# Performance work log

Measured on AMD Instinct MI355X. Metric: run time of the kernel, lower is better.

## Reference

```python
import jax, jax.numpy as jnp
import numpy as np

N_NODES = 25000
N_EDGES = 400000
N_GRAPHS = 64
F_IN = 128


def setup_inputs() -> dict:
    key = jax.random.key(0)
    ks = jax.random.split(key, 16)
    inp = {}
    inp["x"] = jax.random.normal(ks[0], (N_NODES, F_IN), dtype=jnp.float32)
    inp["edge_index"] = jax.random.randint(ks[1], (2, N_EDGES), 0, N_NODES, dtype=jnp.int64)
    inp["edge_attr"] = jax.random.uniform(ks[2], (N_EDGES,), dtype=jnp.float32)
    inp["batch_ids"] = jnp.sort(jax.random.randint(ks[3], (N_NODES,), 0, N_GRAPHS, dtype=jnp.int64))
    def lin(k, fan_in, fan_out):
        bound = 1.0 / np.sqrt(fan_in)
        return jax.random.uniform(k, (fan_in, fan_out), dtype=jnp.float32, minval=-bound, maxval=bound)
    inp["W1_rel"] = lin(ks[4], F_IN, 512)
    inp["b1"] = jnp.zeros((512,), jnp.float32)
    inp["W1_root"] = lin(ks[5], F_IN, 512)
    inp["W2_rel"] = lin(ks[6], 512, 512)
    inp["b2"] = jnp.zeros((512,), jnp.float32)
    inp["W2_root"] = lin(ks[7], 512, 512)
    inp["Wl1"] = lin(ks[8], 512, 64)
    inp["bl1"] = jnp.zeros((64,), jnp.float32)
    inp["Wl2"] = lin(ks[9], 64, 16)
    inp["bl2"] = jnp.zeros((16,), jnp.float32)
    inp["Wl3"] = lin(ks[10], 16, 1)
    inp["bl3"] = jnp.zeros((1,), jnp.float32)
    return inp


def _graph_conv(h, src, dst, edge_attr, W_rel, b_rel, W_root, n_nodes):
    # PyG GraphConv: lin_rel(scatter_add(w_e * x_src, dst)) + lin_root(x)
    msg = h[src] * edge_attr[:, None]                       # [E, F] gather
    agg = jax.ops.segment_sum(msg, dst, num_segments=n_nodes)  # [N, F] scatter-add
    return agg @ W_rel + b_rel + h @ W_root


def reference(x, edge_index, edge_attr, batch_ids, W1_rel, b1, W1_root,
              W2_rel, b2, W2_root, Wl1, bl1, Wl2, bl2, Wl3, bl3):
    n_nodes = x.shape[0]
    src, dst = edge_index[0], edge_index[1]
    h = jax.nn.relu(_graph_conv(x, src, dst, edge_attr, W1_rel, b1, W1_root, n_nodes))
    h = jax.nn.relu(_graph_conv(h, src, dst, edge_attr, W2_rel, b2, W2_root, n_nodes))
    # global mean pool by graph id
    sums = jax.ops.segment_sum(h, batch_ids, num_segments=N_GRAPHS)  # [G, 512]
    counts = jax.ops.segment_sum(jnp.ones((n_nodes,), h.dtype), batch_ids, num_segments=N_GRAPHS)
    g = sums / jnp.maximum(counts, 1.0)[:, None]
    # dropout is identity in eval mode
    g = jax.nn.relu(g @ Wl1 + bl1)
    g = jax.nn.relu(g @ Wl2 + bl2)
    return g @ Wl3 + bl3  # [G, 1]
```

## Files before the change

### kernel.cpp

```cpp
#include <hip/hip_runtime.h>
#include <hip/hip_bf16.h>
#include <hip/hip_fp16.h>
#include <stdint.h>

#define N_NODESC 25000
#define N_EDGESC 400000
#define N_GRAPHSC 64
#define F_INC 128
#define HIDC 512
#define PSTRIDE 1600000

typedef __attribute__((ext_vector_type(8))) short short8;
typedef __attribute__((ext_vector_type(4))) float f32x4;

__device__ __forceinline__ float bf2f(unsigned short u) {
  return __uint_as_float(((unsigned)u) << 16);
}
__device__ __forceinline__ unsigned short f2bf(float f) {
  unsigned u = __float_as_uint(f);
  u += 0x7fffu + ((u >> 16) & 1u);
  return (unsigned short)(u >> 16);
}

__global__ void prep_kernel(const float* __restrict__ x, unsigned short* __restrict__ xp,
                            int* __restrict__ deg, float* __restrict__ gsum) {
  int blk = blockIdx.x, t = threadIdx.x;
  if (blk < 98) {
    int i = blk * 256 + t;
    if (i < N_NODESC) deg[i] = 0;
  } else if (blk < 3223) {
    int idx = ((blk - 98) * 256 + t) * 4;
    int node = idx >> 7;
    int col = idx & 127;
    float4 v = *(const float4*)(x + idx);
    ushort4 o;
    o.x = f2bf(v.x); o.y = f2bf(v.y); o.z = f2bf(v.z); o.w = f2bf(v.w);
    *(ushort4*)(xp + (size_t)(col >> 6) * PSTRIDE + (size_t)node * 64 + (col & 63)) = o;
  } else {
    int i = (blk - 3223) * 256 + t;
    if (i < N_GRAPHSC * HIDC) gsum[i] = 0.f;
  }
}

__global__ __launch_bounds__(256)
void wt_kernel(const float* __restrict__ W1rel, const float* __restrict__ W1root,
               const float* __restrict__ W2rel, const float* __restrict__ W2root,
               unsigned short* __restrict__ W1T, unsigned short* __restrict__ W2T) {
  __shared__ float tile[64][65];
  int blk = blockIdx.x;
  const float* src;
  unsigned short* dst;
  int n0, k0, Kout;
  if (blk < 128) {
    int kt = blk >> 3, nt = blk & 7;
    k0 = kt * 64; n0 = nt * 64;
    src = (k0 < 512) ? (W2rel + (size_t)k0 * 512) : (W2root + (size_t)(k0 - 512) * 512);
    dst = W2T; Kout = 1024;
  } else {
    int b = blk - 128;
    int kt = b >> 3, nt = b & 7;
    k0 = kt * 64; n0 = nt * 64;
    src = (k0 < 128) ? (W1rel + (size_t)k0 * 512) : (W1root + (size_t)(k0 - 128) * 512);
    dst = W1T; Kout = 256;
  }
  int c = threadIdx.x & 63;
  int r4 = threadIdx.x >> 6;
#pragma unroll
  for (int rr = 0; rr < 64; rr += 4) {
    int row = rr + r4;
    tile[c][row] = src[(size_t)row * 512 + n0 + c];
  }
  __syncthreads();
#pragma unroll
  for (int rr = 0; rr < 64; rr += 4) {
    int nrow = rr + r4;
    dst[(size_t)(n0 + nrow) * Kout + k0 + c] = f2bf(tile[nrow][c]);
  }
}

__global__ void deg_kernel(const int* __restrict__ ei, int* __restrict__ deg) {
  int e = blockIdx.x * blockDim.x + threadIdx.x;
  if (e >= N_EDGESC) return;
  atomicAdd(&deg[ei[N_EDGESC + e]], 1);
}

__global__ __launch_bounds__(1024)
void scan_kernel(const int* __restrict__ deg, int* __restrict__ indptr, int* __restrict__ cursor) {
  __shared__ int sums[1024];
  const int t = threadIdx.x;
  const int CH = (N_NODESC + 1023) / 1024;
  const int base = t * CH;
  int s = 0;
  for (int i = 0; i < CH; ++i) {
    int idx = base + i;
    if (idx < N_NODESC) s += deg[idx];
  }
  sums[t] = s;
  __syncthreads();
  for (int off = 1; off < 1024; off <<= 1) {
    int v = (t >= off) ? sums[t - off] : 0;
    __syncthreads();
    sums[t] += v;
    __syncthreads();
  }
  int run = (t > 0) ? sums[t - 1] : 0;
  for (int i = 0; i < CH; ++i) {
    int idx = base + i;
    if (idx < N_NODESC) {
      indptr[idx] = run;
      cursor[idx] = run;
      run += deg[idx];
    }
  }
  if (t == 0) indptr[N_NODESC] = sums[1023];
}

__global__ void fill_kernel(const int* __restrict__ ei, const float* __restrict__ ea,
                            int* __restrict__ cursor, unsigned* __restrict__ emeta) {
  int e = blockIdx.x * blockDim.x + threadIdx.x;
  if (e >= N_EDGESC) return;
  int dst = ei[N_EDGESC + e];
  int pos = atomicAdd(&cursor[dst], 1);
  unsigned short hw = __half_as_ushort(__float2half_rn(ea[e]));
  emeta[pos] = (unsigned)ei[e] | ((unsigned)hw << 16);
}

__global__ __launch_bounds__(256)
void agg_gather_p(const unsigned short* __restrict__ srcfeat, const int* __restrict__ indptr,
                  const unsigned* __restrict__ emeta, unsigned short* __restrict__ outp,
                  int lgP) {
  int P1 = (1 << lgP) - 1;
  int panel = blockIdx.x & P1;
  int node = (blockIdx.x >> lgP) * 4 + (threadIdx.x >> 6);
  if (node >= N_NODESC) return;
  int lane = threadIdx.x & 63;
  int q = lane >> 4;
  int c16 = lane & 15;
  int beg = indptr[node], end = indptr[node + 1];
  const unsigned short* fb = srcfeat + (size_t)panel * PSTRIDE + c16 * 4;
  float a0 = 0.f, a1 = 0.f, a2 = 0.f, a3 = 0.f;
  for (int b = beg; b < end; b += 64) {
    int cnt = end - b;
    if (cnt > 64) cnt = 64;
    unsigned mj = (lane < cnt) ? emeta[b + lane] : 0u;
    for (int j = 0; j < cnt; j += 8) {
      unsigned m0 = __shfl(mj, j + q);
      unsigned m1 = __shfl(mj, j + 4 + q);
      uint2 v0 = *(const uint2*)(fb + (size_t)(m0 & 0xffffu) * 64);
      uint2 v1 = *(const uint2*)(fb + (size_t)(m1 & 0xffffu) * 64);
      float w0 = __half2float(__ushort_as_half((unsigned short)(m0 >> 16)));
      float w1 = __half2float(__ushort_as_half((unsigned short)(m1 >> 16)));
      a0 += __uint_as_float(v0.x << 16) * w0;
      a1 += __uint_as_float(v0.x & 0xffff0000u) * w0;
      a2 += __uint_as_float(v0.y << 16) * w0;
      a3 += __uint_as_float(v0.y & 0xffff0000u) * w0;
      a0 += __uint_as_float(v1.x << 16) * w1;
      a1 += __uint_as_float(v1.x & 0xffff0000u) * w1;
      a2 += __uint_as_float(v1.y << 16) * w1;
      a3 += __uint_as_float(v1.y & 0xffff0000u) * w1;
    }
  }
  a0 += __shfl_xor(a0, 16); a1 += __shfl_xor(a1, 16);
  a2 += __shfl_xor(a2, 16); a3 += __shfl_xor(a3, 16);
  a0 += __shfl_xor(a0, 32); a1 += __shfl_xor(a1, 32);
  a2 += __shfl_xor(a2, 32); a3 += __shfl_xor(a3, 32);
  if (q == 0) {
    ushort4 o;
    o.x = f2bf(a0); o.y = f2bf(a1); o.z = f2bf(a2); o.w = f2bf(a3);
    *(ushort4*)(outp + (size_t)panel * PSTRIDE + (size_t)node * 64 + c16 * 4) = o;
  }
}

__global__ __launch_bounds__(256, 3)
void gemm_bt_relu(const short* __restrict__ A0, const short* __restrict__ A1,
                  const short* __restrict__ BT, const float* __restrict__ bias,
                  unsigned short* __restrict__ Outp, int M, int S) {
  const int K = 2 * S;
  __shared__ __align__(16) short As[128 * 64];
  __shared__ __align__(16) short Bs[128 * 64];
  const int m0 = blockIdx.x * 128;
  const int n0 = blockIdx.y * 128;
  const int tid = threadIdx.x;
  const int wave = tid >> 6;
  const int lane = tid & 63;
  const int quad = lane >> 4;
  const int r = lane & 15;
  const int wm = (wave >> 1) * 64;
  const int wn = (wave & 1) * 64;

  f32x4 acc[4][4] = {};

  const int nk = K >> 6;
  for (int kt = 0; kt < nk; ++kt) {
    const int kbase = kt << 6;
    const short* Ab;
    int koff;
    if (kbase < S) { Ab = A0; koff = kbase; } else { Ab = A1; koff = kbase - S; }
    const short* Apan = Ab + (size_t)(koff >> 6) * PSTRIDE;
#pragma unroll
    for (int i = 0; i < 4; ++i) {
      int s = ((wave * 4 + i) << 6) + lane;
      int row = s >> 3;
      int c = (s & 7) ^ (row & 7);
      int rg = m0 + row; if (rg > M - 1) rg = M - 1;
      const short* gp = Apan + (size_t)rg * 64 + (c << 3);
      __builtin_amdgcn_global_load_lds((const __attribute__((address_space(1))) void*)gp,
                                       (__attribute__((address_space(3))) void*)&As[(wave * 4 + i) * 512],
                                       16, 0, 0);
    }
#pragma unroll
    for (int i = 0; i < 4; ++i) {
      int s = ((wave * 4 + i) << 6) + lane;
      int row = s >> 3;
      int c = (s & 7) ^ (row & 7);
      const short* gp = BT + (size_t)(n0 + row) * K + kbase + (c << 3);
      __builtin_amdgcn_global_load_lds((const __attribute__((address_space(1))) void*)gp,
                                       (__attribute__((address_space(3))) void*)&Bs[(wave * 4 + i) * 512],
                                       16, 0, 0);
    }
    __syncthreads();
#pragma unroll
    for (int ks = 0; ks < 2; ++ks) {
      short8 af[4], bfr[4];
#pragma unroll
      for (int tm = 0; tm < 4; ++tm) {
        int ml = wm + tm * 16 + r;
        int c = (ks << 2) + quad;
        int slot = ml * 8 + (c ^ (ml & 7));
        af[tm] = *(const short8*)&As[slot * 8];
      }
#pragma unroll
      for (int tn = 0; tn < 4; ++tn) {
        int nl = wn + tn * 16 + r;
        int c = (ks << 2) + quad;
        int slot = nl * 8 + (c ^ (nl & 7));
        bfr[tn] = *(const short8*)&Bs[slot * 8];
      }
#pragma unroll
      for (int tm = 0; tm < 4; ++tm)
#pragma unroll
        for (int tn = 0; tn < 4; ++tn)
          acc[tm][tn] = __builtin_amdgcn_mfma_f32_16x16x32_bf16(af[tm], bfr[tn], acc[tm][tn], 0, 0, 0);
    }
    __syncthreads();
  }

#pragma unroll
  for (int tm = 0; tm < 4; ++tm) {
    int rowb = m0 + wm + tm * 16 + quad * 4;
#pragma unroll
    for (int tn = 0; tn < 4; ++tn) {
      int col = n0 + wn + tn * 16 + r;
      float bv = bias[col];
      unsigned short* obase = Outp + (size_t)(col >> 6) * PSTRIDE + (col & 63);
#pragma unroll
      for (int reg = 0; reg < 4; ++reg) {
        int rr = rowb + reg;
        if (rr < M) {
          float v = acc[tm][tn][reg] + bv;
          v = v > 0.f ? v : 0.f;
          obase[(size_t)rr * 64] = f2bf(v);
        }
      }
    }
  }
}

__global__ __launch_bounds__(256, 3)
void gemm_bt_pool(const short* __restrict__ A0, const short* __restrict__ A1,
                  const short* __restrict__ BT, const float* __restrict__ bias,
                  const int* __restrict__ batch, float* __restrict__ gsum, int M, int S) {
  const int K = 2 * S;
  __shared__ __align__(16) short As[128 * 64];
  __shared__ __align__(16) short Bs[128 * 64];
  const int m0 = blockIdx.x * 128;
  const int n0 = blockIdx.y * 128;
  const int tid = threadIdx.x;
  const int wave = tid >> 6;
  const int lane = tid & 63;
  const int quad = lane >> 4;
  const int r = lane & 15;
  const int wm = (wave >> 1) * 64;
  const int wn = (wave & 1) * 64;

  f32x4 acc[4][4] = {};

  const int nk = K >> 6;
  for (int kt = 0; kt < nk; ++kt) {
    const int kbase = kt << 6;
    const short* Ab;
    int koff;
    if (kbase < S) { Ab = A0; koff = kbase; } else { Ab = A1; koff = kbase - S; }
    const short* Apan = Ab + (size_t)(koff >> 6) * PSTRIDE;
#pragma unroll
    for (int i = 0; i < 4; ++i) {
      int s = ((wave * 4 + i) << 6) + lane;
      int row = s >> 3;
      int c = (s & 7) ^ (row & 7);
      int rg = m0 + row; if (rg > M - 1) rg = M - 1;
      const short* gp = Apan + (size_t)rg * 64 + (c << 3);
      __builtin_amdgcn_global_load_lds((const __attribute__((address_space(1))) void*)gp,
                                       (__attribute__((address_space(3))) void*)&As[(wave * 4 + i) * 512],
                                       16, 0, 0);
    }
#pragma unroll
    for (int i = 0; i < 4; ++i) {
      int s = ((wave * 4 + i) << 6) + lane;
      int row = s >> 3;
      int c = (s & 7) ^ (row & 7);
      const short* gp = BT + (size_t)(n0 + row) * K + kbase + (c << 3);
      __builtin_amdgcn_global_load_lds((const __attribute__((address_space(1))) void*)gp,
                                       (__attribute__((address_space(3))) void*)&Bs[(wave * 4 + i) * 512],
                                       16, 0, 0);
    }
    __syncthreads();
#pragma unroll
    for (int ks = 0; ks < 2; ++ks) {
      short8 af[4], bfr[4];
#pragma unroll
      for (int tm = 0; tm < 4; ++tm) {
        int ml = wm + tm * 16 + r;
        int c = (ks << 2) + quad;
        int slot = ml * 8 + (c ^ (ml & 7));
        af[tm] = *(const short8*)&As[slot * 8];
      }
#pragma unroll
      for (int tn = 0; tn < 4; ++tn) {
        int nl = wn + tn * 16 + r;
        int c = (ks << 2) + quad;
        int slot = nl * 8 + (c ^ (nl & 7));
        bfr[tn] = *(const short8*)&Bs[slot * 8];
      }
#pragma unroll
      for (int tm = 0; tm < 4; ++tm)
#pragma unroll
        for (int tn = 0; tn < 4; ++tn)
          acc[tm][tn] = __builtin_amdgcn_mfma_f32_16x16x32_bf16(af[tm], bfr[tn], acc[tm][tn], 0, 0, 0);
    }
    __syncthreads();
  }

  int gid[4][4];
#pragma unroll
  for (int tm = 0; tm < 4; ++tm) {
    int rowb = m0 + wm + tm * 16 + quad * 4;
#pragma unroll
    for (int reg = 0; reg < 4; ++reg) {
      int rr = rowb + reg;
      gid[tm][reg] = batch[rr < M ? rr : (M - 1)];
    }
#pragma unroll
    for (int tn = 0; tn < 4; ++tn) {
      float bv = bias[n0 + wn + tn * 16 + r];
#pragma unroll
      for (int reg = 0; reg < 4; ++reg) {
        int rr = rowb + reg;
        float v = acc[tm][tn][reg] + bv;
        v = v > 0.f ? v : 0.f;
        acc[tm][tn][reg] = (rr < M) ? v : 0.f;
      }
    }
  }
  int g_lo = batch[m0 < M ? m0 : (M - 1)];
  int g_hi = batch[(m0 + 127) < M ? (m0 + 127) : (M - 1)];
  for (int g = g_lo; g <= g_hi; ++g) {
#pragma unroll
    for (int tn = 0; tn < 4; ++tn) {
      float s = 0.f;
#pragma unroll
      for (int tm = 0; tm < 4; ++tm)
#pragma unroll
        for (int reg = 0; reg < 4; ++reg)
          s += (gid[tm][reg] == g) ? acc[tm][tn][reg] : 0.f;
      s += __shfl_xor(s, 16);
      s += __shfl_xor(s, 32);
      if (quad == 0)
        atomicAdd(&gsum[(size_t)g * HIDC + n0 + wn + tn * 16 + r], s);
    }
  }
}

__global__ __launch_bounds__(256)
void mlp_kernel(const float* __restrict__ gsum, const int* __restrict__ batch,
                const float* __restrict__ Wl1, const float* __restrict__ bl1,
                const float* __restrict__ Wl2, const float* __restrict__ bl2,
                const float* __restrict__ Wl3, const float* __restrict__ bl3,
                float* __restrict__ out) {
  int gi = blockIdx.x;
  int t = threadIdx.x;
  int unit = t & 63;
  int part = t >> 6;
  __shared__ float red[4][64];
  __shared__ float h1s[64];
  __shared__ float h2s[16];
  int lo = 0, hi = N_NODESC;
  while (lo < hi) { int mid = (lo + hi) >> 1; if (batch[mid] < gi) lo = mid + 1; else hi = mid; }
  int start = lo;
  hi = N_NODESC;
  while (lo < hi) { int mid = (lo + hi) >> 1; if (batch[mid] < gi + 1) lo = mid + 1; else hi = mid; }
  float inv = 1.0f / fmaxf((float)(lo - start), 1.0f);
  const float* gr = gsum + gi * HIDC;
  float acc = 0.f;
  for (int j = part * 128; j < (part + 1) * 128; ++j)
    acc += gr[j] * Wl1[j * 64 + unit];
  red[part][unit] = acc;
  __syncthreads();
  if (t < 64) {
    float a = bl1[t] + (red[0][t] + red[1][t] + red[2][t] + red[3][t]) * inv;
    h1s[t] = fmaxf(a, 0.f);
  }
  __syncthreads();
  if (t < 16) {
    float a = bl2[t];
    for (int j = 0; j < 64; ++j) a += h1s[j] * Wl2[j * 16 + t];
    h2s[t] = fmaxf(a, 0.f);
  }
  __syncthreads();
  if (t == 0) {
    float a = bl3[0];
    for (int j = 0; j < 16; ++j) a += h2s[j] * Wl3[j];
    out[gi] = a;
  }
}

extern "C" void kernel_launch(void* const* d_in, const int* in_sizes, int n_in,
                              void* d_out, int out_size, void* d_ws, size_t ws_size,
                              hipStream_t stream) {
  const float* x      = (const float*)d_in[0];
  const int*   ei     = (const int*)d_in[1];
  const float* ea     = (const float*)d_in[2];
  const int*   batch  = (const int*)d_in[3];
  const float* W1rel  = (const float*)d_in[4];
  const float* b1     = (const float*)d_in[5];
  const float* W1root = (const float*)d_in[6];
  const float* W2rel  = (const float*)d_in[7];
  const float* b2     = (const float*)d_in[8];
  const float* W2root = (const float*)d_in[9];
  const float* Wl1    = (const float*)d_in[10];
  const float* bl1    = (const float*)d_in[11];
  const float* Wl2    = (const float*)d_in[12];
  const float* bl2    = (const float*)d_in[13];
  const float* Wl3    = (const float*)d_in[14];
  const float* bl3    = (const float*)d_in[15];
  float* out = (float*)d_out;

  char* ws = (char*)d_ws;
  unsigned short* xp     = (unsigned short*)(ws + 0);
  unsigned short* agg1p  = (unsigned short*)(ws + 6400000);
  unsigned short* h1p    = (unsigned short*)(ws + 12800000);
  unsigned short* agg2p  = (unsigned short*)(ws + 38400000);
  unsigned short* W1T    = (unsigned short*)(ws + 64000000);
  unsigned short* W2T    = (unsigned short*)(ws + 64262144);
  float*          gsum   = (float*)(ws + 65310720);
  int*            deg    = (int*)(ws + 65441792);
  int*            cursor = (int*)(ws + 65541792);
  int*            indptr = (int*)(ws + 65641792);
  unsigned*       emeta  = (unsigned*)(ws + 65741808);

  prep_kernel<<<3351, 256, 0, stream>>>(x, xp, deg, gsum);
  wt_kernel<<<160, 256, 0, stream>>>(W1rel, W1root, W2rel, W2root, W1T, W2T);
  deg_kernel<<<(N_EDGESC + 255) / 256, 256, 0, stream>>>(ei, deg);
  scan_kernel<<<1, 1024, 0, stream>>>(deg, indptr, cursor);
  fill_kernel<<<(N_EDGESC + 255) / 256, 256, 0, stream>>>(ei, ea, cursor, emeta);

  agg_gather_p<<<((N_NODESC + 3) / 4) * 2, 256, 0, stream>>>(xp, indptr, emeta, agg1p, 1);

  dim3 gg((N_NODESC + 127) / 128, 4);
  gemm_bt_relu<<<gg, 256, 0, stream>>>((const short*)agg1p, (const short*)xp,
                                       (const short*)W1T, b1, h1p, N_NODESC, 128);

  agg_gather_p<<<((N_NODESC + 3) / 4) * 8, 256, 0, stream>>>(h1p, indptr, emeta, agg2p, 3);

  gemm_bt_pool<<<gg, 256, 0, stream>>>((const short*)agg2p, (const short*)h1p,
                                       (const short*)W2T, b2, batch, gsum, N_NODESC, 512);

  mlp_kernel<<<N_GRAPHSC, 256, 0, stream>>>(gsum, batch, Wl1, bl1, Wl2, bl2, Wl3, bl3, out);
}
```

Measured before the change: 332.0 us.

## Pad CSR rows to multiples of four and load edge metadata directly

New measurement: 340.7 us. 2.6% more time.

```diff
diff --git a/kernel.cpp b/kernel.cpp
--- a/kernel.cpp
+++ b/kernel.cpp
@@ -9,6 +9,7 @@
 #define F_INC 128
 #define HIDC 512
 #define PSTRIDE 1600000
+#define EMETA_CAP 475008
 
 typedef __attribute__((ext_vector_type(8))) short short8;
 typedef __attribute__((ext_vector_type(4))) float f32x4;
@@ -93,7 +94,7 @@
   int s = 0;
   for (int i = 0; i < CH; ++i) {
     int idx = base + i;
-    if (idx < N_NODESC) s += deg[idx];
+    if (idx < N_NODESC) s += (deg[idx] + 3) & ~3;
   }
   sums[t] = s;
   __syncthreads();
@@ -109,7 +110,7 @@
     if (idx < N_NODESC) {
       indptr[idx] = run;
       cursor[idx] = run;
-      run += deg[idx];
+      run += (deg[idx] + 3) & ~3;
     }
   }
   if (t == 0) indptr[N_NODESC] = sums[1023];
@@ -129,36 +130,42 @@
 void agg_gather_p(const unsigned short* __restrict__ srcfeat, const int* __restrict__ indptr,
                   const unsigned* __restrict__ emeta, unsigned short* __restrict__ outp,
                   int lgP) {
-  int P1 = (1 << lgP) - 1;
-  int panel = blockIdx.x & P1;
+  int panel = blockIdx.x & ((1 << lgP) - 1);
   int node = (blockIdx.x >> lgP) * 4 + (threadIdx.x >> 6);
   if (node >= N_NODESC) return;
   int lane = threadIdx.x & 63;
   int q = lane >> 4;
   int c16 = lane & 15;
   int beg = indptr[node], end = indptr[node + 1];
+  int degp = end - beg;
+  const unsigned* mp = emeta + beg + q;
   const unsigned short* fb = srcfeat + (size_t)panel * PSTRIDE + c16 * 4;
   float a0 = 0.f, a1 = 0.f, a2 = 0.f, a3 = 0.f;
-  for (int b = beg; b < end; b += 64) {
-    int cnt = end - b;
-    if (cnt > 64) cnt = 64;
-    unsigned mj = (lane < cnt) ? emeta[b + lane] : 0u;
-    for (int j = 0; j < cnt; j += 8) {
-      unsigned m0 = __shfl(mj, j + q);
-      unsigned m1 = __shfl(mj, j + 4 + q);
-      uint2 v0 = *(const uint2*)(fb + (size_t)(m0 & 0xffffu) * 64);
-      uint2 v1 = *(const uint2*)(fb + (size_t)(m1 & 0xffffu) * 64);
-      float w0 = __half2float(__ushort_as_half((unsigned short)(m0 >> 16)));
-      float w1 = __half2float(__ushort_as_half((unsigned short)(m1 >> 16)));
-      a0 += __uint_as_float(v0.x << 16) * w0;
-      a1 += __uint_as_float(v0.x & 0xffff0000u) * w0;
-      a2 += __uint_as_float(v0.y << 16) * w0;
-      a3 += __uint_as_float(v0.y & 0xffff0000u) * w0;
-      a0 += __uint_as_float(v1.x << 16) * w1;
-      a1 += __uint_as_float(v1.x & 0xffff0000u) * w1;
-      a2 += __uint_as_float(v1.y << 16) * w1;
-      a3 += __uint_as_float(v1.y & 0xffff0000u) * w1;
-    }
+  int j = 0;
+  for (; j + 8 <= degp; j += 8) {
+    unsigned mA = mp[j];
+    unsigned mB = mp[j + 4];
+    uint2 vA = *(const uint2*)(fb + (size_t)(mA & 0xffffu) * 64);
+    uint2 vB = *(const uint2*)(fb + (size_t)(mB & 0xffffu) * 64);
+    float wA = __half2float(__ushort_as_half((unsigned short)(mA >> 16)));
+    float wB = __half2float(__ushort_as_half((unsigned short)(mB >> 16)));
+    a0 += __uint_as_float(vA.x << 16) * wA;
+    a1 += __uint_as_float(vA.x & 0xffff0000u) * wA;
+    a2 += __uint_as_float(vA.y << 16) * wA;
+    a3 += __uint_as_float(vA.y & 0xffff0000u) * wA;
+    a0 += __uint_as_float(vB.x << 16) * wB;
+    a1 += __uint_as_float(vB.x & 0xffff0000u) * wB;
+    a2 += __uint_as_float(vB.y << 16) * wB;
+    a3 += __uint_as_float(vB.y & 0xffff0000u) * wB;
+  }
+  if (j < degp) {
+    unsigned mA = mp[j];
+    uint2 vA = *(const uint2*)(fb + (size_t)(mA & 0xffffu) * 64);
+    float wA = __half2float(__ushort_as_half((unsigned short)(mA >> 16)));
+    a0 += __uint_as_float(vA.x << 16) * wA;
+    a1 += __uint_as_float(vA.x & 0xffff0000u) * wA;
+    a2 += __uint_as_float(vA.y << 16) * wA;
+    a3 += __uint_as_float(vA.y & 0xffff0000u) * wA;
   }
   a0 += __shfl_xor(a0, 16); a1 += __shfl_xor(a1, 16);
   a2 += __shfl_xor(a2, 16); a3 += __shfl_xor(a3, 16);
@@ -460,6 +467,7 @@
   prep_kernel<<<3351, 256, 0, stream>>>(x, xp, deg, gsum);
   wt_kernel<<<160, 256, 0, stream>>>(W1rel, W1root, W2rel, W2root, W1T, W2T);
   deg_kernel<<<(N_EDGESC + 255) / 256, 256, 0, stream>>>(ei, deg);
+  hipMemsetAsync(emeta, 0, EMETA_CAP * sizeof(unsigned), stream);
   scan_kernel<<<1, 1024, 0, stream>>>(deg, indptr, cursor);
   fill_kernel<<<(N_EDGESC + 255) / 256, 256, 0, stream>>>(ei, ea, cursor, emeta);
 
```
